# Optimization experiments

Hardware: AMD Instinct MI355X
Metric: run time of the kernel (lower is better)

Reference implementation:

```python
import jax, jax.numpy as jnp
import numpy as np

N_NODES = 50000
N_EDGES = 800000
N_GRAPHS = 128
IN_C, HID_C, OUT_C = 128, 256, 128


def setup_inputs() -> dict:
    key = jax.random.key(0)
    ks = jax.random.split(key, 10)
    x = jax.random.normal(ks[0], (N_NODES, IN_C), dtype=jnp.float32)
    edge_index = jax.random.randint(ks[1], (2, N_EDGES), 0, N_NODES, dtype=jnp.int32)
    batch = jnp.sort(jax.random.randint(ks[2], (N_NODES,), 0, N_GRAPHS, dtype=jnp.int32))
    def glorot(k, fan_in, fan_out):
        lim = (6.0 / (fan_in + fan_out)) ** 0.5
        return jax.random.uniform(k, (fan_in, fan_out), jnp.float32, -lim, lim)
    W1 = glorot(ks[3], IN_C, HID_C)
    b1 = jnp.zeros((HID_C,), jnp.float32)
    W2 = glorot(ks[4], HID_C, HID_C)
    b2 = jnp.zeros((HID_C,), jnp.float32)
    Wfc = glorot(ks[5], HID_C, OUT_C)
    bfc = jnp.zeros((OUT_C,), jnp.float32)
    return {"x": x, "edge_index": edge_index, "batch": batch,
            "W1": W1, "b1": b1, "W2": W2, "b2": b2, "Wfc": Wfc, "bfc": bfc}


def _gcn_conv(x, src, dst, W, b, n_nodes):
    # PyG GCNConv: h = x @ W; out[dst] += norm * h[src]; out += b
    h = x @ W  # [N, F_out]
    ones = jnp.ones(src.shape, dtype=h.dtype)
    deg = jax.ops.segment_sum(ones, dst, num_segments=n_nodes)  # in-degree incl self loops
    dinv = jnp.where(deg > 0, jax.lax.rsqrt(deg), 0.0)
    norm = dinv[src] * dinv[dst]                    # [E]
    msg = h[src] * norm[:, None]                    # gather + scale, [E, F_out]
    out = jax.ops.segment_sum(msg, dst, num_segments=n_nodes)  # scatter-add
    return out + b


def reference(x, edge_index, batch, W1, b1, W2, b2, Wfc, bfc):
    n = x.shape[0]
    loops = jnp.arange(n, dtype=edge_index.dtype)
    src = jnp.concatenate([edge_index[0], loops])   # add self loops (GCNConv default)
    dst = jnp.concatenate([edge_index[1], loops])
    h = jax.nn.relu(_gcn_conv(x, src, dst, W1, b1, n))
    h = jax.nn.relu(_gcn_conv(h, src, dst, W2, b2, n))
    # global_mean_pool keyed by batch index
    sums = jax.ops.segment_sum(h, batch, num_segments=N_GRAPHS)          # [G, HID]
    cnts = jax.ops.segment_sum(jnp.ones((n,), h.dtype), batch, num_segments=N_GRAPHS)
    pooled = sums / jnp.maximum(cnts, 1.0)[:, None]
    return pooled @ Wfc + bfc
```

## Files before the change

kernel.cpp:

```cpp
#include <hip/hip_runtime.h>
#include <type_traits>

#define HID 256
#define INC 128
#define OUTC 128

typedef __attribute__((ext_vector_type(8))) short short8;
typedef __attribute__((ext_vector_type(4))) float floatx4;

__device__ __forceinline__ unsigned short f2bf(float f) {
    unsigned int u = __float_as_uint(f);
    unsigned int r = (u + 0x7FFFu + ((u >> 16) & 1u)) >> 16;
    return (unsigned short)r;
}

__device__ __forceinline__ void bfacc2(float* a, uint u, float nr) {
    a[0] = fmaf(nr, __uint_as_float(u << 16), a[0]);
    a[1] = fmaf(nr, __uint_as_float(u & 0xFFFF0000u), a[1]);
}

__global__ void k_convX(const float* __restrict__ x, unsigned short* __restrict__ xb, int total4) {
    int i = blockIdx.x * 256 + threadIdx.x;
    if (i < total4) {
        const float4 v = *(const float4*)(x + (size_t)i * 4);
        uint2 o;
        o.x = (unsigned)f2bf(v.x) | ((unsigned)f2bf(v.y) << 16);
        o.y = (unsigned)f2bf(v.z) | ((unsigned)f2bf(v.w) << 16);
        *(uint2*)(xb + (size_t)i * 4) = o;
    }
}

__global__ void k_hist(const int* __restrict__ dst, int* __restrict__ cnt, int e) {
    int i = blockIdx.x * blockDim.x + threadIdx.x;
    if (i < e) atomicAdd(&cnt[dst[i]], 1);
}

__global__ __launch_bounds__(256) void k_scan_local(const int* __restrict__ cnt,
                                                    int* __restrict__ ex, int* __restrict__ blk_sum,
                                                    float* __restrict__ dinv, int n) {
    __shared__ int s[256];
    const int t = threadIdx.x;
    const int i = blockIdx.x * 256 + t;
    const int v = (i < n) ? cnt[i] : 0;
    if (i < n) dinv[i] = rsqrtf((float)v + 1.0f);
    s[t] = v;
    __syncthreads();
    for (int off = 1; off < 256; off <<= 1) {
        int add = (t >= off) ? s[t - off] : 0;
        __syncthreads();
        s[t] += add;
        __syncthreads();
    }
    if (i < n) ex[i] = s[t] - v;
    if (t == 255) blk_sum[blockIdx.x] = s[255];
}

__global__ __launch_bounds__(256) void k_scan_add(int* __restrict__ row_ptr,
                                                  const int* __restrict__ blk_sum,
                                                  int* __restrict__ cnt, int n, int e) {
    __shared__ int s[256];
    const int t = threadIdx.x;
    const int b = blockIdx.x;
    s[t] = (t < b) ? blk_sum[t] : 0;
    __syncthreads();
    for (int off = 128; off > 0; off >>= 1) {
        if (t < off) s[t] += s[t + off];
        __syncthreads();
    }
    const int offset = s[0];
    const int i = b * 256 + t;
    if (i < n) { row_ptr[i] += offset; cnt[i] = 0; }
    if (i == 0) row_ptr[n] = e;
}

__global__ void k_fill(const int* __restrict__ src, const int* __restrict__ dst,
                       const int* __restrict__ row_ptr, int* __restrict__ cursor,
                       int* __restrict__ csr_src, float* __restrict__ csr_nrm,
                       const float* __restrict__ dinv, int e) {
    int i = blockIdx.x * blockDim.x + threadIdx.x;
    if (i < e) {
        const int d = dst[i];
        const int s = src[i];
        const int pos = row_ptr[d] + atomicAdd(&cursor[d], 1);
        csr_src[pos] = s;
        csr_nrm[pos] = dinv[s] * dinv[d];
    }
}

__global__ void k_convW(const float* __restrict__ W1, unsigned short* __restrict__ Wt1,
                        const float* __restrict__ W2, unsigned short* __restrict__ Wt2) {
    int id = blockIdx.x * 256 + threadIdx.x;
    if (id < INC * HID) {
        int n = id / INC;
        int k = id - n * INC;
        Wt1[id] = f2bf(W1[k * HID + n]);
    } else if (id < INC * HID + HID * HID) {
        int id2 = id - INC * HID;
        int n = id2 / HID;
        int k = id2 - n * HID;
        Wt2[id2] = f2bf(W2[k * HID + n]);
    }
}

template <int CH>
__global__ __launch_bounds__(256) void k_agg(const unsigned short* __restrict__ h,
                                             const int* __restrict__ row_ptr,
                                             const int* __restrict__ csr_src,
                                             const float* __restrict__ csr_nrm,
                                             const float* __restrict__ dinv,
                                             unsigned short* __restrict__ out, int n) {
    constexpr int CPL = CH / 64;
    using VT = std::conditional_t<CPL == 2, uint, uint2>;
    const int v = (blockIdx.x * 256 + threadIdx.x) >> 6;
    const int lane = threadIdx.x & 63;
    if (v >= n) return;
    const float dv = dinv[v];
    const unsigned short* hl = h + lane * CPL;

    float acc[CPL];
    {
        const VT u = *(const VT*)(hl + (size_t)v * CH);
        const float s2 = dv * dv;
        if constexpr (CPL == 2) {
            acc[0] = s2 * __uint_as_float(((uint)u) << 16);
            acc[1] = s2 * __uint_as_float(((uint)u) & 0xFFFF0000u);
        } else {
            const uint2 w = (uint2)u;
            acc[0] = s2 * __uint_as_float(w.x << 16);
            acc[1] = s2 * __uint_as_float(w.x & 0xFFFF0000u);
            acc[2] = s2 * __uint_as_float(w.y << 16);
            acc[3] = s2 * __uint_as_float(w.y & 0xFFFF0000u);
        }
    }

    const int beg = row_ptr[v];
    const int end = row_ptr[v + 1];
    int i = beg;
    for (; i + 4 <= end; i += 4) {
        const int s0 = csr_src[i];
        const int s1 = csr_src[i + 1];
        const int s2i = csr_src[i + 2];
        const int s3 = csr_src[i + 3];
        const float n0 = csr_nrm[i];
        const float n1 = csr_nrm[i + 1];
        const float n2 = csr_nrm[i + 2];
        const float n3 = csr_nrm[i + 3];
        const VT r0 = *(const VT*)(hl + (size_t)s0 * CH);
        const VT r1 = *(const VT*)(hl + (size_t)s1 * CH);
        const VT r2 = *(const VT*)(hl + (size_t)s2i * CH);
        const VT r3 = *(const VT*)(hl + (size_t)s3 * CH);
        if constexpr (CPL == 2) {
            bfacc2(acc, (uint)r0, n0);
            bfacc2(acc, (uint)r1, n1);
            bfacc2(acc, (uint)r2, n2);
            bfacc2(acc, (uint)r3, n3);
        } else {
            const uint2 w0 = (uint2)r0, w1 = (uint2)r1, w2 = (uint2)r2, w3 = (uint2)r3;
            bfacc2(acc, w0.x, n0); bfacc2(acc + 2, w0.y, n0);
            bfacc2(acc, w1.x, n1); bfacc2(acc + 2, w1.y, n1);
            bfacc2(acc, w2.x, n2); bfacc2(acc + 2, w2.y, n2);
            bfacc2(acc, w3.x, n3); bfacc2(acc + 2, w3.y, n3);
        }
    }
    for (; i < end; ++i) {
        const int s0 = csr_src[i];
        const float n0 = csr_nrm[i];
        const VT r0 = *(const VT*)(hl + (size_t)s0 * CH);
        if constexpr (CPL == 2) {
            bfacc2(acc, (uint)r0, n0);
        } else {
            const uint2 w0 = (uint2)r0;
            bfacc2(acc, w0.x, n0); bfacc2(acc + 2, w0.y, n0);
        }
    }

    if constexpr (CPL == 2) {
        uint o = (unsigned)f2bf(acc[0]) | ((unsigned)f2bf(acc[1]) << 16);
        *(uint*)(out + (size_t)v * CH + lane * CPL) = o;
    } else {
        uint2 o;
        o.x = (unsigned)f2bf(acc[0]) | ((unsigned)f2bf(acc[1]) << 16);
        o.y = (unsigned)f2bf(acc[2]) | ((unsigned)f2bf(acc[3]) << 16);
        *(uint2*)(out + (size_t)v * CH + lane * CPL) = o;
    }
}

template <int K, bool RELU, bool POOL, typename OT>
__global__ __launch_bounds__(256) void k_gemm_mfma(const unsigned short* __restrict__ A,
                                                   const unsigned short* __restrict__ Wt,
                                                   const float* __restrict__ bias,
                                                   OT* __restrict__ out,
                                                   const int* __restrict__ batch,
                                                   float* __restrict__ pooled_sum, int M) {
    constexpr int LDA = K + 8;
    __shared__ unsigned short sA[32 * LDA];
    __shared__ int s_batch[32];
    const int t = threadIdx.x;
    const int row0 = blockIdx.x * 32;

    {
        const int r = t >> 3;
        const int c0 = (t & 7) * (K / 8);
        unsigned short* dstp = &sA[r * LDA + c0];
        if (row0 + r < M) {
            const unsigned short* srcp = A + (size_t)(row0 + r) * K + c0;
#pragma unroll
            for (int j = 0; j < K / 8; j += 8)
                *(uint4*)(dstp + j) = *(const uint4*)(srcp + j);
        } else {
            const uint4 z = {0, 0, 0, 0};
#pragma unroll
            for (int j = 0; j < K / 8; j += 8) *(uint4*)(dstp + j) = z;
        }
        if constexpr (POOL) {
            if (t < 32) s_batch[t] = (row0 + t < M) ? batch[row0 + t] : -1;
        }
    }
    __syncthreads();

    const int wv = t >> 6;
    const int lane = t & 63;
    const int m16 = lane & 15;
    const int quad = lane >> 4;

    floatx4 acc[2][4];
#pragma unroll
    for (int h2 = 0; h2 < 2; ++h2)
#pragma unroll
        for (int j = 0; j < 4; ++j) acc[h2][j] = (floatx4){0.f, 0.f, 0.f, 0.f};

    const unsigned short* ap0 = &sA[m16 * LDA + quad * 8];
    const unsigned short* ap1 = &sA[(16 + m16) * LDA + quad * 8];
    const unsigned short* bp = Wt + (size_t)(wv * 64 + m16) * K + quad * 8;

#pragma unroll
    for (int k0 = 0; k0 < K; k0 += 32) {
        const short8 a0 = *(const short8*)(ap0 + k0);
        const short8 a1 = *(const short8*)(ap1 + k0);
        const short8 b0 = *(const short8*)(bp + 0 * 16 * K + k0);
        const short8 b1 = *(const short8*)(bp + 1 * 16 * K + k0);
        const short8 b2 = *(const short8*)(bp + 2 * 16 * K + k0);
        const short8 b3 = *(const short8*)(bp + 3 * 16 * K + k0);
        acc[0][0] = __builtin_amdgcn_mfma_f32_16x16x32_bf16(a0, b0, acc[0][0], 0, 0, 0);
        acc[0][1] = __builtin_amdgcn_mfma_f32_16x16x32_bf16(a0, b1, acc[0][1], 0, 0, 0);
        acc[0][2] = __builtin_amdgcn_mfma_f32_16x16x32_bf16(a0, b2, acc[0][2], 0, 0, 0);
        acc[0][3] = __builtin_amdgcn_mfma_f32_16x16x32_bf16(a0, b3, acc[0][3], 0, 0, 0);
        acc[1][0] = __builtin_amdgcn_mfma_f32_16x16x32_bf16(a1, b0, acc[1][0], 0, 0, 0);
        acc[1][1] = __builtin_amdgcn_mfma_f32_16x16x32_bf16(a1, b1, acc[1][1], 0, 0, 0);
        acc[1][2] = __builtin_amdgcn_mfma_f32_16x16x32_bf16(a1, b2, acc[1][2], 0, 0, 0);
        acc[1][3] = __builtin_amdgcn_mfma_f32_16x16x32_bf16(a1, b3, acc[1][3], 0, 0, 0);
    }

    const int nbase = wv * 64 + m16;
    const float bb0 = bias[nbase + 0];
    const float bb1 = bias[nbase + 16];
    const float bb2 = bias[nbase + 32];
    const float bb3 = bias[nbase + 48];

    if constexpr (POOL) {
        float ps0 = 0.f, ps1 = 0.f, ps2 = 0.f, ps3 = 0.f;
        int gcur = -1;
#pragma unroll
        for (int h2 = 0; h2 < 2; ++h2) {
#pragma unroll
            for (int j = 0; j < 4; ++j) {
                const int rl = h2 * 16 + quad * 4 + j;
                const int g = s_batch[rl];
                if (g < 0) continue;
                if (g != gcur) {
                    if (gcur >= 0) {
                        float* pp = pooled_sum + gcur * HID + nbase;
                        atomicAdd(pp + 0, ps0);
                        atomicAdd(pp + 16, ps1);
                        atomicAdd(pp + 32, ps2);
                        atomicAdd(pp + 48, ps3);
                    }
                    ps0 = ps1 = ps2 = ps3 = 0.f;
                    gcur = g;
                }
                ps0 += fmaxf(acc[h2][0][j] + bb0, 0.f);
                ps1 += fmaxf(acc[h2][1][j] + bb1, 0.f);
                ps2 += fmaxf(acc[h2][2][j] + bb2, 0.f);
                ps3 += fmaxf(acc[h2][3][j] + bb3, 0.f);
            }
        }
        if (gcur >= 0) {
            float* pp = pooled_sum + gcur * HID + nbase;
            atomicAdd(pp + 0, ps0);
            atomicAdd(pp + 16, ps1);
            atomicAdd(pp + 32, ps2);
            atomicAdd(pp + 48, ps3);
        }
    } else {
#pragma unroll
        for (int h2 = 0; h2 < 2; ++h2) {
#pragma unroll
            for (int j = 0; j < 4; ++j) {
                const int row = row0 + h2 * 16 + quad * 4 + j;
                if (row >= M) continue;
                float v0 = acc[h2][0][j] + bb0;
                float v1 = acc[h2][1][j] + bb1;
                float v2 = acc[h2][2][j] + bb2;
                float v3 = acc[h2][3][j] + bb3;
                if constexpr (RELU) {
                    v0 = fmaxf(v0, 0.f); v1 = fmaxf(v1, 0.f);
                    v2 = fmaxf(v2, 0.f); v3 = fmaxf(v3, 0.f);
                }
                out[(size_t)row * HID + nbase + 0]  = (OT)f2bf(v0);
                out[(size_t)row * HID + nbase + 16] = (OT)f2bf(v1);
                out[(size_t)row * HID + nbase + 32] = (OT)f2bf(v2);
                out[(size_t)row * HID + nbase + 48] = (OT)f2bf(v3);
            }
        }
    }
}

__global__ void k_fc(const float* __restrict__ pooled_sum, const int* __restrict__ batch,
                     const float* __restrict__ W, const float* __restrict__ b,
                     float* __restrict__ out, int n) {
    const int g = blockIdx.x;
    const int c = threadIdx.x;
    int a = 0, hi = n;
    while (a < hi) { int m = (a + hi) >> 1; if (batch[m] < g) a = m + 1; else hi = m; }
    const int start = a;
    hi = n;
    while (a < hi) { int m = (a + hi) >> 1; if (batch[m] < g + 1) a = m + 1; else hi = m; }
    const float cnt = (float)(a - start);

    float acc = 0.0f;
    const float* p = pooled_sum + g * HID;
    for (int k = 0; k < HID; ++k) acc += p[k] * W[k * OUTC + c];
    out[g * OUTC + c] = acc / fmaxf(cnt, 1.0f) + b[c];
}

extern "C" void kernel_launch(void* const* d_in, const int* in_sizes, int n_in,
                              void* d_out, int out_size, void* d_ws, size_t ws_size,
                              hipStream_t stream) {
    const float* x   = (const float*)d_in[0];
    const int*   ei  = (const int*)d_in[1];
    const int*   bat = (const int*)d_in[2];
    const float* W1  = (const float*)d_in[3];
    const float* b1  = (const float*)d_in[4];
    const float* W2  = (const float*)d_in[5];
    const float* b2  = (const float*)d_in[6];
    const float* Wfc = (const float*)d_in[7];
    const float* bfc = (const float*)d_in[8];
    float* out = (float*)d_out;

    const int n = in_sizes[2];
    const int e = in_sizes[1] / 2;
    const int* src = ei;
    const int* dst = ei + e;
    const int nb = (n + 255) / 256;

    size_t off = 0;
    auto alloc = [&](size_t bytes) {
        char* p = (char*)d_ws + off;
        off += (bytes + 255) & ~(size_t)255;
        return p;
    };
    int*   cnt     = (int*)alloc((size_t)n * 4);
    int*   row_ptr = (int*)alloc((size_t)(n + 1) * 4);
    int*   blk_sum = (int*)alloc(512 * 4);
    int*   csr_src = (int*)alloc((size_t)e * 4);
    float* csr_nrm = (float*)alloc((size_t)e * 4);
    float* dinv    = (float*)alloc((size_t)n * 4);
    unsigned short* Wt1 = (unsigned short*)alloc((size_t)INC * HID * 2);
    unsigned short* Wt2 = (unsigned short*)alloc((size_t)HID * HID * 2);
    unsigned short* R1  = (unsigned short*)alloc((size_t)n * HID * 2);
    unsigned short* R2  = (unsigned short*)alloc((size_t)n * INC * 2);
    unsigned short* R3  = (unsigned short*)alloc((size_t)n * HID * 2);
    float* pooled = (float*)alloc((size_t)128 * HID * 4);

    const int TB = 256;
    hipMemsetAsync(cnt, 0, (size_t)n * 4, stream);
    hipMemsetAsync(pooled, 0, (size_t)128 * HID * 4, stream);

    k_convX<<<((n * INC / 4) + TB - 1) / TB, TB, 0, stream>>>(x, R1, n * INC / 4);

    k_hist<<<(e + TB - 1) / TB, TB, 0, stream>>>(dst, cnt, e);
    k_scan_local<<<nb, TB, 0, stream>>>(cnt, row_ptr, blk_sum, dinv, n);
    k_scan_add<<<nb, TB, 0, stream>>>(row_ptr, blk_sum, cnt, n, e);
    k_fill<<<(e + TB - 1) / TB, TB, 0, stream>>>(src, dst, row_ptr, cnt, csr_src, csr_nrm, dinv, e);

    k_convW<<<(INC * HID + HID * HID + TB - 1) / TB, TB, 0, stream>>>(W1, Wt1, W2, Wt2);

    const int gemm_blocks = (n + 31) / 32;
    const int agg_blocks = (n + 3) / 4;

    k_agg<INC><<<agg_blocks, TB, 0, stream>>>(R1, row_ptr, csr_src, csr_nrm, dinv, R2, n);
    k_gemm_mfma<INC, true, false, unsigned short><<<gemm_blocks, TB, 0, stream>>>(
        R2, Wt1, b1, R3, nullptr, nullptr, n);

    k_agg<HID><<<agg_blocks, TB, 0, stream>>>(R3, row_ptr, csr_src, csr_nrm, dinv, R1, n);
    k_gemm_mfma<HID, true, true, float><<<gemm_blocks, TB, 0, stream>>>(
        R1, Wt2, b2, (float*)nullptr, bat, pooled, n);

    k_fc<<<128, 128, 0, stream>>>(pooled, bat, Wfc, bfc, out, n);
}
```

Before: 351.8 us.

## Fuse sparse aggregation into MFMA GEMM and merge conversion kernels

Sparse neighbour aggregation and the dense MFMA GEMM are merged into one kernel. Each block aggregates 32 rows straight into shared memory and then multiplies them by the weights, so the bf16 intermediate no longer makes a round trip through global memory. The x and weight conversion kernels are also merged into one launch. In exchange, each block now has only 32 rows of gather parallelism (8 rows per wave, processed serially). This may reduce memory-level parallelism and latency hiding compared with the one-wave-per-node aggregation kernel.

```diff
diff --git a/kernel.cpp b/kernel.cpp
--- a/kernel.cpp
+++ b/kernel.cpp
@@ -17,17 +17,6 @@
 __device__ __forceinline__ void bfacc2(float* a, uint u, float nr) {
     a[0] = fmaf(nr, __uint_as_float(u << 16), a[0]);
     a[1] = fmaf(nr, __uint_as_float(u & 0xFFFF0000u), a[1]);
-}
-
-__global__ void k_convX(const float* __restrict__ x, unsigned short* __restrict__ xb, int total4) {
-    int i = blockIdx.x * 256 + threadIdx.x;
-    if (i < total4) {
-        const float4 v = *(const float4*)(x + (size_t)i * 4);
-        uint2 o;
-        o.x = (unsigned)f2bf(v.x) | ((unsigned)f2bf(v.y) << 16);
-        o.y = (unsigned)f2bf(v.z) | ((unsigned)f2bf(v.w) << 16);
-        *(uint2*)(xb + (size_t)i * 4) = o;
-    }
 }
 
 __global__ void k_hist(const int* __restrict__ dst, int* __restrict__ cnt, int e) {
@@ -87,139 +76,133 @@
     }
 }
 
-__global__ void k_convW(const float* __restrict__ W1, unsigned short* __restrict__ Wt1,
-                        const float* __restrict__ W2, unsigned short* __restrict__ Wt2) {
+__global__ void k_conv(const float* __restrict__ x, unsigned short* __restrict__ xb,
+                       const float* __restrict__ W1, unsigned short* __restrict__ Wt1,
+                       const float* __restrict__ W2, unsigned short* __restrict__ Wt2, int nx4) {
     int id = blockIdx.x * 256 + threadIdx.x;
-    if (id < INC * HID) {
-        int n = id / INC;
-        int k = id - n * INC;
-        Wt1[id] = f2bf(W1[k * HID + n]);
-    } else if (id < INC * HID + HID * HID) {
-        int id2 = id - INC * HID;
-        int n = id2 / HID;
-        int k = id2 - n * HID;
-        Wt2[id2] = f2bf(W2[k * HID + n]);
-    }
-}
-
-template <int CH>
-__global__ __launch_bounds__(256) void k_agg(const unsigned short* __restrict__ h,
-                                             const int* __restrict__ row_ptr,
-                                             const int* __restrict__ csr_src,
-                                             const float* __restrict__ csr_nrm,
-                                             const float* __restrict__ dinv,
-                                             unsigned short* __restrict__ out, int n) {
-    constexpr int CPL = CH / 64;
+    if (id < nx4) {
+        const float4 v = *(const float4*)(x + (size_t)id * 4);
+        uint2 o;
+        o.x = (unsigned)f2bf(v.x) | ((unsigned)f2bf(v.y) << 16);
+        o.y = (unsigned)f2bf(v.z) | ((unsigned)f2bf(v.w) << 16);
+        *(uint2*)(xb + (size_t)id * 4) = o;
+        return;
+    }
+    int id2 = id - nx4;
+    if (id2 < INC * HID) {
+        const int nn = id2 / INC;
+        const int kk = id2 - nn * INC;
+        Wt1[id2] = f2bf(W1[kk * HID + nn]);
+        return;
+    }
+    int id3 = id2 - INC * HID;
+    if (id3 < HID * HID) {
+        const int nn = id3 / HID;
+        const int kk = id3 - nn * HID;
+        Wt2[id3] = f2bf(W2[kk * HID + nn]);
+    }
+}
+
+template <int K, bool POOL>
+__global__ __launch_bounds__(256) void k_agg_gemm(const unsigned short* __restrict__ h,
+                                                  const int* __restrict__ row_ptr,
+                                                  const int* __restrict__ csr_src,
+                                                  const float* __restrict__ csr_nrm,
+                                                  const float* __restrict__ dinv,
+                                                  const unsigned short* __restrict__ Wt,
+                                                  const float* __restrict__ bias,
+                                                  unsigned short* __restrict__ out,
+                                                  const int* __restrict__ batch,
+                                                  float* __restrict__ pooled_sum, int M) {
+    constexpr int LDA = K + 8;
+    constexpr int CPL = K / 64;
     using VT = std::conditional_t<CPL == 2, uint, uint2>;
-    const int v = (blockIdx.x * 256 + threadIdx.x) >> 6;
-    const int lane = threadIdx.x & 63;
-    if (v >= n) return;
-    const float dv = dinv[v];
-    const unsigned short* hl = h + lane * CPL;
-
-    float acc[CPL];
-    {
-        const VT u = *(const VT*)(hl + (size_t)v * CH);
-        const float s2 = dv * dv;
-        if constexpr (CPL == 2) {
-            acc[0] = s2 * __uint_as_float(((uint)u) << 16);
-            acc[1] = s2 * __uint_as_float(((uint)u) & 0xFFFF0000u);
-        } else {
-            const uint2 w = (uint2)u;
-            acc[0] = s2 * __uint_as_float(w.x << 16);
-            acc[1] = s2 * __uint_as_float(w.x & 0xFFFF0000u);
-            acc[2] = s2 * __uint_as_float(w.y << 16);
-            acc[3] = s2 * __uint_as_float(w.y & 0xFFFF0000u);
-        }
-    }
-
-    const int beg = row_ptr[v];
-    const int end = row_ptr[v + 1];
-    int i = beg;
-    for (; i + 4 <= end; i += 4) {
-        const int s0 = csr_src[i];
-        const int s1 = csr_src[i + 1];
-        const int s2i = csr_src[i + 2];
-        const int s3 = csr_src[i + 3];
-        const float n0 = csr_nrm[i];
-        const float n1 = csr_nrm[i + 1];
-        const float n2 = csr_nrm[i + 2];
-        const float n3 = csr_nrm[i + 3];
-        const VT r0 = *(const VT*)(hl + (size_t)s0 * CH);
-        const VT r1 = *(const VT*)(hl + (size_t)s1 * CH);
-        const VT r2 = *(const VT*)(hl + (size_t)s2i * CH);
-        const VT r3 = *(const VT*)(hl + (size_t)s3 * CH);
-        if constexpr (CPL == 2) {
-            bfacc2(acc, (uint)r0, n0);
-            bfacc2(acc, (uint)r1, n1);
-            bfacc2(acc, (uint)r2, n2);
-            bfacc2(acc, (uint)r3, n3);
-        } else {
-            const uint2 w0 = (uint2)r0, w1 = (uint2)r1, w2 = (uint2)r2, w3 = (uint2)r3;
-            bfacc2(acc, w0.x, n0); bfacc2(acc + 2, w0.y, n0);
-            bfacc2(acc, w1.x, n1); bfacc2(acc + 2, w1.y, n1);
-            bfacc2(acc, w2.x, n2); bfacc2(acc + 2, w2.y, n2);
-            bfacc2(acc, w3.x, n3); bfacc2(acc + 2, w3.y, n3);
-        }
-    }
-    for (; i < end; ++i) {
-        const int s0 = csr_src[i];
-        const float n0 = csr_nrm[i];
-        const VT r0 = *(const VT*)(hl + (size_t)s0 * CH);
-        if constexpr (CPL == 2) {
-            bfacc2(acc, (uint)r0, n0);
-        } else {
-            const uint2 w0 = (uint2)r0;
-            bfacc2(acc, w0.x, n0); bfacc2(acc + 2, w0.y, n0);
-        }
-    }
-
-    if constexpr (CPL == 2) {
-        uint o = (unsigned)f2bf(acc[0]) | ((unsigned)f2bf(acc[1]) << 16);
-        *(uint*)(out + (size_t)v * CH + lane * CPL) = o;
-    } else {
-        uint2 o;
-        o.x = (unsigned)f2bf(acc[0]) | ((unsigned)f2bf(acc[1]) << 16);
-        o.y = (unsigned)f2bf(acc[2]) | ((unsigned)f2bf(acc[3]) << 16);
-        *(uint2*)(out + (size_t)v * CH + lane * CPL) = o;
-    }
-}
-
-template <int K, bool RELU, bool POOL, typename OT>
-__global__ __launch_bounds__(256) void k_gemm_mfma(const unsigned short* __restrict__ A,
-                                                   const unsigned short* __restrict__ Wt,
-                                                   const float* __restrict__ bias,
-                                                   OT* __restrict__ out,
-                                                   const int* __restrict__ batch,
-                                                   float* __restrict__ pooled_sum, int M) {
-    constexpr int LDA = K + 8;
     __shared__ unsigned short sA[32 * LDA];
     __shared__ int s_batch[32];
     const int t = threadIdx.x;
+    const int w = t >> 6;
+    const int lane = t & 63;
     const int row0 = blockIdx.x * 32;
 
-    {
-        const int r = t >> 3;
-        const int c0 = (t & 7) * (K / 8);
-        unsigned short* dstp = &sA[r * LDA + c0];
-        if (row0 + r < M) {
-            const unsigned short* srcp = A + (size_t)(row0 + r) * K + c0;
-#pragma unroll
-            for (int j = 0; j < K / 8; j += 8)
-                *(uint4*)(dstp + j) = *(const uint4*)(srcp + j);
+    const unsigned short* hl = h + lane * CPL;
+    for (int j = 0; j < 8; ++j) {
+        const int r = w * 8 + j;
+        const int v = row0 + r;
+        float acc[CPL];
+#pragma unroll
+        for (int c = 0; c < CPL; ++c) acc[c] = 0.f;
+        if (v < M) {
+            const float dv = dinv[v];
+            {
+                const VT u = *(const VT*)(hl + (size_t)v * K);
+                const float s2 = dv * dv;
+                if constexpr (CPL == 2) {
+                    acc[0] = s2 * __uint_as_float(((uint)u) << 16);
+                    acc[1] = s2 * __uint_as_float(((uint)u) & 0xFFFF0000u);
+                } else {
+                    const uint2 q = (uint2)u;
+                    acc[0] = s2 * __uint_as_float(q.x << 16);
+                    acc[1] = s2 * __uint_as_float(q.x & 0xFFFF0000u);
+                    acc[2] = s2 * __uint_as_float(q.y << 16);
+                    acc[3] = s2 * __uint_as_float(q.y & 0xFFFF0000u);
+                }
+            }
+            const int beg = row_ptr[v];
+            const int end = row_ptr[v + 1];
+            int i = beg;
+            for (; i + 4 <= end; i += 4) {
+                const int s0 = csr_src[i];
+                const int s1 = csr_src[i + 1];
+                const int s2i = csr_src[i + 2];
+                const int s3 = csr_src[i + 3];
+                const float n0 = csr_nrm[i];
+                const float n1 = csr_nrm[i + 1];
+                const float n2 = csr_nrm[i + 2];
+                const float n3 = csr_nrm[i + 3];
+                const VT r0 = *(const VT*)(hl + (size_t)s0 * K);
+                const VT r1 = *(const VT*)(hl + (size_t)s1 * K);
+                const VT r2 = *(const VT*)(hl + (size_t)s2i * K);
+                const VT r3 = *(const VT*)(hl + (size_t)s3 * K);
+                if constexpr (CPL == 2) {
+                    bfacc2(acc, (uint)r0, n0);
+                    bfacc2(acc, (uint)r1, n1);
+                    bfacc2(acc, (uint)r2, n2);
+                    bfacc2(acc, (uint)r3, n3);
+                } else {
+                    const uint2 q0 = (uint2)r0, q1 = (uint2)r1, q2 = (uint2)r2, q3 = (uint2)r3;
+                    bfacc2(acc, q0.x, n0); bfacc2(acc + 2, q0.y, n0);
+                    bfacc2(acc, q1.x, n1); bfacc2(acc + 2, q1.y, n1);
+                    bfacc2(acc, q2.x, n2); bfacc2(acc + 2, q2.y, n2);
+                    bfacc2(acc, q3.x, n3); bfacc2(acc + 2, q3.y, n3);
+                }
+            }
+            for (; i < end; ++i) {
+                const int s0 = csr_src[i];
+                const float n0 = csr_nrm[i];
+                const VT r0 = *(const VT*)(hl + (size_t)s0 * K);
+                if constexpr (CPL == 2) {
+                    bfacc2(acc, (uint)r0, n0);
+                } else {
+                    const uint2 q0 = (uint2)r0;
+                    bfacc2(acc, q0.x, n0); bfacc2(acc + 2, q0.y, n0);
+                }
+            }
+        }
+        if constexpr (CPL == 2) {
+            uint o = (unsigned)f2bf(acc[0]) | ((unsigned)f2bf(acc[1]) << 16);
+            *(uint*)(&sA[r * LDA + lane * 2]) = o;
         } else {
-            const uint4 z = {0, 0, 0, 0};
-#pragma unroll
-            for (int j = 0; j < K / 8; j += 8) *(uint4*)(dstp + j) = z;
-        }
-        if constexpr (POOL) {
-            if (t < 32) s_batch[t] = (row0 + t < M) ? batch[row0 + t] : -1;
-        }
+            uint2 o;
+            o.x = (unsigned)f2bf(acc[0]) | ((unsigned)f2bf(acc[1]) << 16);
+            o.y = (unsigned)f2bf(acc[2]) | ((unsigned)f2bf(acc[3]) << 16);
+            *(uint2*)(&sA[r * LDA + lane * 4]) = o;
+        }
+    }
+    if constexpr (POOL) {
+        if (t < 32) s_batch[t] = (row0 + t < M) ? batch[row0 + t] : -1;
     }
     __syncthreads();
 
-    const int wv = t >> 6;
-    const int lane = t & 63;
     const int m16 = lane & 15;
     const int quad = lane >> 4;
 
@@ -231,7 +214,7 @@
 
     const unsigned short* ap0 = &sA[m16 * LDA + quad * 8];
     const unsigned short* ap1 = &sA[(16 + m16) * LDA + quad * 8];
-    const unsigned short* bp = Wt + (size_t)(wv * 64 + m16) * K + quad * 8;
+    const unsigned short* bp = Wt + (size_t)(w * 64 + m16) * K + quad * 8;
 
 #pragma unroll
     for (int k0 = 0; k0 < K; k0 += 32) {
@@ -251,7 +234,7 @@
         acc[1][3] = __builtin_amdgcn_mfma_f32_16x16x32_bf16(a1, b3, acc[1][3], 0, 0, 0);
     }
 
-    const int nbase = wv * 64 + m16;
+    const int nbase = w * 64 + m16;
     const float bb0 = bias[nbase + 0];
     const float bb1 = bias[nbase + 16];
     const float bb2 = bias[nbase + 32];
@@ -298,18 +281,10 @@
             for (int j = 0; j < 4; ++j) {
                 const int row = row0 + h2 * 16 + quad * 4 + j;
                 if (row >= M) continue;
-                float v0 = acc[h2][0][j] + bb0;
-                float v1 = acc[h2][1][j] + bb1;
-                float v2 = acc[h2][2][j] + bb2;
-                float v3 = acc[h2][3][j] + bb3;
-                if constexpr (RELU) {
-                    v0 = fmaxf(v0, 0.f); v1 = fmaxf(v1, 0.f);
-                    v2 = fmaxf(v2, 0.f); v3 = fmaxf(v3, 0.f);
-                }
-                out[(size_t)row * HID + nbase + 0]  = (OT)f2bf(v0);
-                out[(size_t)row * HID + nbase + 16] = (OT)f2bf(v1);
-                out[(size_t)row * HID + nbase + 32] = (OT)f2bf(v2);
-                out[(size_t)row * HID + nbase + 48] = (OT)f2bf(v3);
+                out[(size_t)row * HID + nbase + 0]  = f2bf(fmaxf(acc[h2][0][j] + bb0, 0.f));
+                out[(size_t)row * HID + nbase + 16] = f2bf(fmaxf(acc[h2][1][j] + bb1, 0.f));
+                out[(size_t)row * HID + nbase + 32] = f2bf(fmaxf(acc[h2][2][j] + bb2, 0.f));
+                out[(size_t)row * HID + nbase + 48] = f2bf(fmaxf(acc[h2][3][j] + bb3, 0.f));
             }
         }
     }
@@ -367,34 +342,30 @@
     float* dinv    = (float*)alloc((size_t)n * 4);
     unsigned short* Wt1 = (unsigned short*)alloc((size_t)INC * HID * 2);
     unsigned short* Wt2 = (unsigned short*)alloc((size_t)HID * HID * 2);
-    unsigned short* R1  = (unsigned short*)alloc((size_t)n * HID * 2);
-    unsigned short* R2  = (unsigned short*)alloc((size_t)n * INC * 2);
+    unsigned short* R1  = (unsigned short*)alloc((size_t)n * INC * 2);
     unsigned short* R3  = (unsigned short*)alloc((size_t)n * HID * 2);
     float* pooled = (float*)alloc((size_t)128 * HID * 4);
 
     const int TB = 256;
+    const int nx4 = n * INC / 4;
     hipMemsetAsync(cnt, 0, (size_t)n * 4, stream);
     hipMemsetAsync(pooled, 0, (size_t)128 * HID * 4, stream);
 
-    k_convX<<<((n * INC / 4) + TB - 1) / TB, TB, 0, stream>>>(x, R1, n * INC / 4);
+    k_conv<<<(nx4 + INC * HID + HID * HID + TB - 1) / TB, TB, 0, stream>>>(
+        x, R1, W1, Wt1, W2, Wt2, nx4);
 
     k_hist<<<(e + TB - 1) / TB, TB, 0, stream>>>(dst, cnt, e);
     k_scan_local<<<nb, TB, 0, stream>>>(cnt, row_ptr, blk_sum, dinv, n);
     k_scan_add<<<nb, TB, 0, stream>>>(row_ptr, blk_sum, cnt, n, e);
     k_fill<<<(e + TB - 1) / TB, TB, 0, stream>>>(src, dst, row_ptr, cnt, csr_src, csr_nrm, dinv, e);
 
-    k_convW<<<(INC * HID + HID * HID + TB - 1) / TB, TB, 0, stream>>>(W1, Wt1, W2, Wt2);
-
-    const int gemm_blocks = (n + 31) / 32;
-    const int agg_blocks = (n + 3) / 4;
-
-    k_agg<INC><<<agg_blocks, TB, 0, stream>>>(R1, row_ptr, csr_src, csr_nrm, dinv, R2, n);
-    k_gemm_mfma<INC, true, false, unsigned short><<<gemm_blocks, TB, 0, stream>>>(
-        R2, Wt1, b1, R3, nullptr, nullptr, n);
-
-    k_agg<HID><<<agg_blocks, TB, 0, stream>>>(R3, row_ptr, csr_src, csr_nrm, dinv, R1, n);
-    k_gemm_mfma<HID, true, true, float><<<gemm_blocks, TB, 0, stream>>>(
-        R1, Wt2, b2, (float*)nullptr, bat, pooled, n);
+    const int blocks = (n + 31) / 32;
+
+    k_agg_gemm<INC, false><<<blocks, TB, 0, stream>>>(
+        R1, row_ptr, csr_src, csr_nrm, dinv, Wt1, b1, R3, nullptr, nullptr, n);
+
+    k_agg_gemm<HID, true><<<blocks, TB, 0, stream>>>(
+        R3, row_ptr, csr_src, csr_nrm, dinv, Wt2, b2, nullptr, bat, pooled, n);
 
     k_fc<<<128, 128, 0, stream>>>(pooled, bat, Wfc, bfc, out, n);
 }
```

New measurement: 383.7 us. 1.09x slower.
